# Kernel optimization log

Measured on AMD Instinct MI355X. Metric: run time of the kernel, lower is better.

Reference implementation:

```python
import jax, jax.numpy as jnp
import numpy as np
from jax import lax

EPS = 1e-5

def setup_inputs() -> dict:
    key = jax.random.key(0)
    k1, k2, k3 = jax.random.split(key, 3)
    B, S, D, W = 4, 4096, 2048, 4
    x = jax.random.normal(k1, (B, S, D), dtype=jnp.float32)
    norm_weight = jnp.ones((D,), dtype=jnp.float32)
    conv_weight = jax.random.normal(k2, (D, W), dtype=jnp.float32) * (1.0 / np.sqrt(W))
    proj_weight = jax.random.normal(k3, (2, D), dtype=jnp.float32) * (1.0 / np.sqrt(D))
    return {"x": x, "norm_weight": norm_weight, "conv_weight": conv_weight, "proj_weight": proj_weight}

def _rmsnorm(x, w):
    var = jnp.mean(x * x, axis=-1, keepdims=True)
    return x * lax.rsqrt(var + EPS) * w

def _causal_dw_conv_silu(h, conv_weight):
    # h: [B,S,D], conv_weight: [D,W]; causal depthwise conv along seq + silu
    B, S, D = h.shape
    W = conv_weight.shape[-1]
    hc = jnp.transpose(h, (0, 2, 1))                      # [B,D,S]
    hc = jnp.pad(hc, ((0, 0), (0, 0), (W - 1, 0)))        # left-pad for causality
    y = lax.conv_general_dilated(
        hc, conv_weight[:, None, :], window_strides=(1,), padding='VALID',
        dimension_numbers=('NCH', 'OIH', 'NCH'), feature_group_count=D)
    return jnp.transpose(jax.nn.silu(y), (0, 2, 1))       # [B,S,D]

def reference(x, norm_weight, conv_weight, proj_weight):
    B, S, D = x.shape
    h = _rmsnorm(x, norm_weight)
    h = _causal_dw_conv_silu(h, conv_weight)
    logits = jnp.einsum('bsd,od->bso', h, proj_weight)    # [B,S,2]
    gate = jax.nn.softmax(logits, axis=-1)[..., 1]        # [B,S]
    mask = gate > 0.5                                     # [B,S]
    # cumsum-index scatter-compress: selected tokens packed to the front,
    # unselected tokens routed to slot 0 which is dropped (padded to S, vs
    # data-dependent max_q in torch).
    idx = jnp.where(mask, jnp.cumsum(mask.astype(jnp.int32), axis=1), 0)  # [B,S]
    buf = jnp.zeros((B, S + 1, D), dtype=x.dtype)
    bidx = jnp.arange(B)[:, None]
    buf = buf.at[bidx, idx].set(x)
    return buf[:, 1:]
```

## Files before the change

### kernel.cpp

```cpp
#include <hip/hip_runtime.h>
#include <cstddef>

#define BATCH 4
#define SEQ   4096
#define DIM   2048
#define EPSF  1e-5f
#define TCHUNK 16
#define CPB   (SEQ / TCHUNK)
#define NBLK  (BATCH * CPB)
#define SROWS 8
#define NSCAT (BATCH * (SEQ / SROWS))

typedef float f4 __attribute__((ext_vector_type(4)));

__device__ __forceinline__ float wave_sum(float v) {
#pragma unroll
    for (int off = 32; off > 0; off >>= 1)
        v += __shfl_down(v, off, 64);
    return v;
}
__device__ __forceinline__ int wave_sum_i(int v) {
#pragma unroll
    for (int off = 32; off > 0; off >>= 1)
        v += __shfl_down(v, off, 64);
    return v;
}

__global__ __launch_bounds__(256, 3) void mask_kernel(
    const float* __restrict__ x, const float* __restrict__ nw,
    const float* __restrict__ cw, const float* __restrict__ pw,
    unsigned int* __restrict__ cnt)
{
    __shared__ float lds_ss[5][4][4];
    __shared__ float lds_acc[4][4][4];

    const int t = threadIdx.x, lane = t & 63, wid = t >> 6;
    const int G = gridDim.x;
    const int chunk = (blockIdx.x & 7) * (G >> 3) + (blockIdx.x >> 3);
    const int b  = chunk / CPB;
    const int s0 = (chunk % CPB) * TCHUNK;
    const int d0 = 4 * t, d1 = d0 + 1024;

    float cwn[8][4], pd[8];
    {
        float4 n0 = *(const float4*)(nw + d0);
        float4 n1 = *(const float4*)(nw + d1);
        float nv[8] = {n0.x, n0.y, n0.z, n0.w, n1.x, n1.y, n1.z, n1.w};
#pragma unroll
        for (int i = 0; i < 8; ++i) {
            const int d = (i < 4) ? (d0 + i) : (d1 + i - 4);
            float4 c4 = *(const float4*)(cw + 4 * d);
            cwn[i][0] = c4.x * nv[i]; cwn[i][1] = c4.y * nv[i];
            cwn[i][2] = c4.z * nv[i]; cwn[i][3] = c4.w * nv[i];
        }
        float4 a0 = *(const float4*)(pw + d0);
        float4 a1 = *(const float4*)(pw + d1);
        float4 b0 = *(const float4*)(pw + DIM + d0);
        float4 b1 = *(const float4*)(pw + DIM + d1);
        pd[0] = b0.x - a0.x; pd[1] = b0.y - a0.y; pd[2] = b0.z - a0.z; pd[3] = b0.w - a0.w;
        pd[4] = b1.x - a1.x; pd[5] = b1.y - a1.y; pd[6] = b1.z - a1.z; pd[7] = b1.w - a1.w;
    }

    const float* xb = x + (size_t)b * SEQ * DIM;
    float h1[8], h2[8], h3[8];

    {
        float wv[3][8];
#pragma unroll
        for (int w = 0; w < 3; ++w) {
            const int s = s0 - 3 + w;
            if (s >= 0) {
                float4 a = *(const float4*)(xb + (size_t)s * DIM + d0);
                float4 c = *(const float4*)(xb + (size_t)s * DIM + d1);
                wv[w][0]=a.x; wv[w][1]=a.y; wv[w][2]=a.z; wv[w][3]=a.w;
                wv[w][4]=c.x; wv[w][5]=c.y; wv[w][6]=c.z; wv[w][7]=c.w;
            } else {
#pragma unroll
                for (int i = 0; i < 8; ++i) wv[w][i] = 0.f;
            }
            float ss = 0.f;
#pragma unroll
            for (int i = 0; i < 8; ++i) ss += wv[w][i] * wv[w][i];
            ss = wave_sum(ss);
            if (lane == 0) lds_ss[4][w][wid] = ss;
        }
        __syncthreads();
#pragma unroll
        for (int w = 0; w < 3; ++w) {
            const float sum4 = lds_ss[4][w][0] + lds_ss[4][w][1]
                             + lds_ss[4][w][2] + lds_ss[4][w][3];
            const float rstd = 1.0f / sqrtf(sum4 * (1.0f / DIM) + EPSF);
            float* h = (w == 0) ? h3 : (w == 1) ? h2 : h1;
#pragma unroll
            for (int i = 0; i < 8; ++i) h[i] = wv[w][i] * rstd;
        }
    }

#pragma unroll
    for (int g = 0; g < 4; ++g) {
        float xv[4][8];
#pragma unroll
        for (int j = 0; j < 4; ++j) {
            const int s = s0 + 4 * g + j;
            float4 a = *(const float4*)(xb + (size_t)s * DIM + d0);
            float4 c = *(const float4*)(xb + (size_t)s * DIM + d1);
            xv[j][0]=a.x; xv[j][1]=a.y; xv[j][2]=a.z; xv[j][3]=a.w;
            xv[j][4]=c.x; xv[j][5]=c.y; xv[j][6]=c.z; xv[j][7]=c.w;
        }
#pragma unroll
        for (int j = 0; j < 4; ++j) {
            float ss = 0.f;
#pragma unroll
            for (int i = 0; i < 8; ++i) ss += xv[j][i] * xv[j][i];
            ss = wave_sum(ss);
            if (lane == 0) lds_ss[g][j][wid] = ss;
        }
        __syncthreads();
#pragma unroll
        for (int j = 0; j < 4; ++j) {
            const float sum4 = lds_ss[g][j][0] + lds_ss[g][j][1]
                             + lds_ss[g][j][2] + lds_ss[g][j][3];
            const float rstd = 1.0f / sqrtf(sum4 * (1.0f / DIM) + EPSF);
            float acc = 0.f;
#pragma unroll
            for (int i = 0; i < 8; ++i) {
                const float hc = xv[j][i] * rstd;
                const float y = cwn[i][0] * h3[i] + cwn[i][1] * h2[i]
                              + cwn[i][2] * h1[i] + cwn[i][3] * hc;
                const float sig = 1.0f / (1.0f + __expf(-y));
                acc += (y * sig) * pd[i];
                h3[i] = h2[i]; h2[i] = h1[i]; h1[i] = hc;
            }
            acc = wave_sum(acc);
            if (lane == 0) lds_acc[g][j][wid] = acc;
        }
    }
    __syncthreads();

    if (wid == 0) {
        int sel = 0;
        if (lane < 16) {
            const int g = lane >> 2, j = lane & 3;
            const float a = lds_acc[g][j][0] + lds_acc[g][j][1]
                          + lds_acc[g][j][2] + lds_acc[g][j][3];
            sel = (a > 0.f) ? 1 : 0;
        }
        const unsigned long long bal = __ballot(sel);
        if (lane == 0)
            cnt[chunk] = (unsigned)__popcll(bal)
                       | ((unsigned)(bal & 0xFFFFull) << 16);
    }
}

__global__ __launch_bounds__(256) void scatter_kernel(
    const float* __restrict__ x, const unsigned int* __restrict__ cnt,
    float* __restrict__ out)
{
    __shared__ unsigned int lds_r[4];
    const int blk  = blockIdx.x;
    const int b    = blk >> 9;
    const int c8   = blk & 511;
    const int mc   = c8 >> 1;
    const int hf   = c8 & 1;
    const int t = threadIdx.x, lane = t & 63, wid = t >> 6;

    const unsigned int* cb = cnt + b * CPB;
    const unsigned vown   = cb[mc];
    const unsigned bits16 = vown >> 16;
    const unsigned bits   = (bits16 >> (8 * hf)) & 0xFFu;

    const unsigned u = cb[t];

    const int s0 = c8 * SROWS;
    const float* xb = x + (size_t)b * SEQ * DIM;
    const int d0 = 4 * t, d1 = d0 + 1024;
    const float4 z = make_float4(0.f, 0.f, 0.f, 0.f);
    float4 ra[SROWS], rc[SROWS];
#pragma unroll
    for (int j = 0; j < SROWS; ++j) {
        if ((bits >> j) & 1) {
            const float* src = xb + (size_t)(s0 + j) * DIM;
            ra[j] = *(const float4*)(src + d0);
            rc[j] = *(const float4*)(src + d1);
        } else { ra[j] = z; rc[j] = z; }
    }

    const int c = (int)(u & 0xFFFFu);
    int pack = ((t < mc) ? c : 0) + (c << 16);
    pack = wave_sum_i(pack);
    if (lane == 0) lds_r[wid] = (unsigned)pack;
    __syncthreads();
    const unsigned tot = lds_r[0] + lds_r[1] + lds_r[2] + lds_r[3];
    const int pre  = (int)(tot & 0xFFFFu)
                   + (hf ? __popc(bits16 & 0xFFu) : 0);
    const int nsel = (int)(tot >> 16);

    float* ob = out + (size_t)b * SEQ * DIM;
#pragma unroll
    for (int j = 0; j < SROWS; ++j) {
        const int incl = __popc(bits & ((2u << j) - 1u));
        const int p    = pre + incl;
        const int sel  = (bits >> j) & 1;
        const int dest = sel ? (p - 1) : (nsel + s0 + j - p);
        float* o = ob + (size_t)dest * DIM;
        __builtin_nontemporal_store(*(const f4*)&ra[j], (f4*)(o + d0));
        __builtin_nontemporal_store(*(const f4*)&rc[j], (f4*)(o + d1));
    }
}

extern "C" void kernel_launch(void* const* d_in, const int* in_sizes, int n_in,
                              void* d_out, int out_size, void* d_ws, size_t ws_size,
                              hipStream_t stream) {
    const float* x  = (const float*)d_in[0];
    const float* nw = (const float*)d_in[1];
    const float* cw = (const float*)d_in[2];
    const float* pw = (const float*)d_in[3];
    float* out = (float*)d_out;

    unsigned int* cnt = (unsigned int*)d_ws;
    mask_kernel<<<NBLK, 256, 0, stream>>>(x, nw, cw, pw, cnt);
    scatter_kernel<<<NSCAT, 256, 0, stream>>>(x, cnt, out);
}
```

Before: 263.2 us.

## Compute all row norms in one pass with a single barrier, then reload rows

```diff
diff --git a/kernel.cpp b/kernel.cpp
--- a/kernel.cpp
+++ b/kernel.cpp
@@ -6,6 +6,7 @@
 #define DIM   2048
 #define EPSF  1e-5f
 #define TCHUNK 16
+#define NROWS (TCHUNK + 3)
 #define CPB   (SEQ / TCHUNK)
 #define NBLK  (BATCH * CPB)
 #define SROWS 8
@@ -31,8 +32,8 @@
     const float* __restrict__ cw, const float* __restrict__ pw,
     unsigned int* __restrict__ cnt)
 {
-    __shared__ float lds_ss[5][4][4];
-    __shared__ float lds_acc[4][4][4];
+    __shared__ float lds_ss[NROWS][4];
+    __shared__ float lds_acc[TCHUNK][4];
 
     const int t = threadIdx.x, lane = t & 63, wid = t >> 6;
     const int G = gridDim.x;
@@ -62,87 +63,73 @@
     }
 
     const float* xb = x + (size_t)b * SEQ * DIM;
+
+    float ssp[NROWS];
+#pragma unroll
+    for (int r = 0; r < NROWS; ++r) {
+        const int s = s0 - 3 + r;
+        float ss = 0.f;
+        if (s >= 0) {
+            const float4 a = *(const float4*)(xb + (size_t)s * DIM + d0);
+            const float4 c = *(const float4*)(xb + (size_t)s * DIM + d1);
+            ss += a.x * a.x; ss += a.y * a.y; ss += a.z * a.z; ss += a.w * a.w;
+            ss += c.x * c.x; ss += c.y * c.y; ss += c.z * c.z; ss += c.w * c.w;
+        }
+        ssp[r] = ss;
+    }
+#pragma unroll
+    for (int r = 0; r < NROWS; ++r) {
+        const float ss = wave_sum(ssp[r]);
+        if (lane == 0) lds_ss[r][wid] = ss;
+    }
+    __syncthreads();
+
     float h1[8], h2[8], h3[8];
-
-    {
-        float wv[3][8];
-#pragma unroll
-        for (int w = 0; w < 3; ++w) {
-            const int s = s0 - 3 + w;
-            if (s >= 0) {
-                float4 a = *(const float4*)(xb + (size_t)s * DIM + d0);
-                float4 c = *(const float4*)(xb + (size_t)s * DIM + d1);
-                wv[w][0]=a.x; wv[w][1]=a.y; wv[w][2]=a.z; wv[w][3]=a.w;
-                wv[w][4]=c.x; wv[w][5]=c.y; wv[w][6]=c.z; wv[w][7]=c.w;
-            } else {
-#pragma unroll
-                for (int i = 0; i < 8; ++i) wv[w][i] = 0.f;
-            }
-            float ss = 0.f;
-#pragma unroll
-            for (int i = 0; i < 8; ++i) ss += wv[w][i] * wv[w][i];
-            ss = wave_sum(ss);
-            if (lane == 0) lds_ss[4][w][wid] = ss;
-        }
-        __syncthreads();
-#pragma unroll
-        for (int w = 0; w < 3; ++w) {
-            const float sum4 = lds_ss[4][w][0] + lds_ss[4][w][1]
-                             + lds_ss[4][w][2] + lds_ss[4][w][3];
-            const float rstd = 1.0f / sqrtf(sum4 * (1.0f / DIM) + EPSF);
-            float* h = (w == 0) ? h3 : (w == 1) ? h2 : h1;
-#pragma unroll
-            for (int i = 0; i < 8; ++i) h[i] = wv[w][i] * rstd;
-        }
-    }
-
-#pragma unroll
-    for (int g = 0; g < 4; ++g) {
-        float xv[4][8];
-#pragma unroll
-        for (int j = 0; j < 4; ++j) {
-            const int s = s0 + 4 * g + j;
-            float4 a = *(const float4*)(xb + (size_t)s * DIM + d0);
-            float4 c = *(const float4*)(xb + (size_t)s * DIM + d1);
-            xv[j][0]=a.x; xv[j][1]=a.y; xv[j][2]=a.z; xv[j][3]=a.w;
-            xv[j][4]=c.x; xv[j][5]=c.y; xv[j][6]=c.z; xv[j][7]=c.w;
-        }
-#pragma unroll
-        for (int j = 0; j < 4; ++j) {
-            float ss = 0.f;
-#pragma unroll
-            for (int i = 0; i < 8; ++i) ss += xv[j][i] * xv[j][i];
-            ss = wave_sum(ss);
-            if (lane == 0) lds_ss[g][j][wid] = ss;
-        }
-        __syncthreads();
-#pragma unroll
-        for (int j = 0; j < 4; ++j) {
-            const float sum4 = lds_ss[g][j][0] + lds_ss[g][j][1]
-                             + lds_ss[g][j][2] + lds_ss[g][j][3];
-            const float rstd = 1.0f / sqrtf(sum4 * (1.0f / DIM) + EPSF);
+#pragma unroll
+    for (int i = 0; i < 8; ++i) { h1[i] = 0.f; h2[i] = 0.f; h3[i] = 0.f; }
+
+#pragma unroll
+    for (int r = 0; r < NROWS; ++r) {
+        const int s = s0 - 3 + r;
+        float v[8];
+        if (s >= 0) {
+            const float4 a = *(const float4*)(xb + (size_t)s * DIM + d0);
+            const float4 c = *(const float4*)(xb + (size_t)s * DIM + d1);
+            v[0]=a.x; v[1]=a.y; v[2]=a.z; v[3]=a.w;
+            v[4]=c.x; v[5]=c.y; v[6]=c.z; v[7]=c.w;
+        } else {
+#pragma unroll
+            for (int i = 0; i < 8; ++i) v[i] = 0.f;
+        }
+        const float sum4 = lds_ss[r][0] + lds_ss[r][1]
+                         + lds_ss[r][2] + lds_ss[r][3];
+        const float rstd = 1.0f / sqrtf(sum4 * (1.0f / DIM) + EPSF);
+        float hc[8];
+#pragma unroll
+        for (int i = 0; i < 8; ++i) hc[i] = v[i] * rstd;
+
+        if (r >= 3) {
             float acc = 0.f;
 #pragma unroll
             for (int i = 0; i < 8; ++i) {
-                const float hc = xv[j][i] * rstd;
                 const float y = cwn[i][0] * h3[i] + cwn[i][1] * h2[i]
-                              + cwn[i][2] * h1[i] + cwn[i][3] * hc;
+                              + cwn[i][2] * h1[i] + cwn[i][3] * hc[i];
                 const float sig = 1.0f / (1.0f + __expf(-y));
                 acc += (y * sig) * pd[i];
-                h3[i] = h2[i]; h2[i] = h1[i]; h1[i] = hc;
             }
             acc = wave_sum(acc);
-            if (lane == 0) lds_acc[g][j][wid] = acc;
-        }
+            if (lane == 0) lds_acc[r - 3][wid] = acc;
+        }
+#pragma unroll
+        for (int i = 0; i < 8; ++i) { h3[i] = h2[i]; h2[i] = h1[i]; h1[i] = hc[i]; }
     }
     __syncthreads();
 
     if (wid == 0) {
         int sel = 0;
-        if (lane < 16) {
-            const int g = lane >> 2, j = lane & 3;
-            const float a = lds_acc[g][j][0] + lds_acc[g][j][1]
-                          + lds_acc[g][j][2] + lds_acc[g][j][3];
+        if (lane < TCHUNK) {
+            const float a = lds_acc[lane][0] + lds_acc[lane][1]
+                          + lds_acc[lane][2] + lds_acc[lane][3];
             sel = (a > 0.f) ? 1 : 0;
         }
         const unsigned long long bal = __ballot(sel);
```

After: 284.9 us. 8.2% more time.
